# Kernel tuning notes

Measured on AMD Instinct MI355X. Metric: run time of the kernel, lower is better.

Reference implementation:

```python
import jax, jax.numpy as jnp
import numpy as np

H = 128          # hid_feats
IN0, IN1 = 128, 64
OUT = 64         # out_feats
L = 3            # num_layers
N = 50000        # nodes per graph


def _rbf(x, W, b):
    # sklearn RBFSampler: z = sqrt(2/D) * cos(x @ W + b)
    return jnp.sqrt(2.0 / H) * jnp.cos(x @ W + b)


def _sage_branch(feat, src, dst, Wself, Wneigh, bias, n_nodes):
    # deg of each dst node (constant across layers)
    deg = jax.ops.segment_sum(jnp.ones_like(dst, dtype=feat.dtype), dst, n_nodes)
    denom = jnp.maximum(deg, 1.0)[:, None]
    for i in range(Wself.shape[0]):
        s = jax.ops.segment_sum(feat[src], dst, n_nodes)   # gather + scatter-add
        neigh = jnp.where(deg[:, None] > 0, s / denom, 0.0)
        feat = feat @ Wself[i] + neigh @ Wneigh[i] + bias[i]
    return feat


def setup_inputs() -> dict:
    key = jax.random.key(0)
    ks = jax.random.split(key, 20)
    gamma = 0.1
    inp = {}
    inp['feat0'] = jax.random.normal(ks[0], (N, IN0), jnp.float32)
    inp['feat1'] = jax.random.normal(ks[1], (N, IN1), jnp.float32)
    E = 800000
    inp['src0'] = jax.random.randint(ks[2], (E,), 0, N, jnp.int32)
    inp['dst0'] = jax.random.randint(ks[3], (E,), 0, N, jnp.int32)
    inp['src1'] = jax.random.randint(ks[4], (E,), 0, N, jnp.int32)
    inp['dst1'] = jax.random.randint(ks[5], (E,), 0, N, jnp.int32)
    # RBF random Fourier feature params (W ~ sqrt(2*gamma)*N(0,1), b ~ U[0,2pi))
    inp['rbf_W0'] = jnp.sqrt(2 * gamma) * jax.random.normal(ks[6], (IN0, H), jnp.float32)
    inp['rbf_b0'] = jax.random.uniform(ks[7], (H,), jnp.float32, 0.0, 2 * np.pi)
    inp['rbf_W1'] = jnp.sqrt(2 * gamma) * jax.random.normal(ks[8], (IN1, H), jnp.float32)
    inp['rbf_b1'] = jax.random.uniform(ks[9], (H,), jnp.float32, 0.0, 2 * np.pi)
    sc = 1.0 / np.sqrt(H)
    # branch 1 (g1) and branch 2 (g0) SAGEConv params, stacked over layers
    inp['Wself1'] = sc * jax.random.normal(ks[10], (L, H, H), jnp.float32)
    inp['Wneigh1'] = sc * jax.random.normal(ks[11], (L, H, H), jnp.float32)
    inp['b1'] = jnp.zeros((L, H), jnp.float32)
    inp['Wself2'] = sc * jax.random.normal(ks[12], (L, H, H), jnp.float32)
    inp['Wneigh2'] = sc * jax.random.normal(ks[13], (L, H, H), jnp.float32)
    inp['b2'] = jnp.zeros((L, H), jnp.float32)
    inp['fc1_W'] = sc * jax.random.normal(ks[14], (2 * H, H), jnp.float32)
    inp['fc1_b'] = jnp.zeros((H,), jnp.float32)
    inp['out_W'] = sc * jax.random.normal(ks[15], (H, OUT), jnp.float32)
    inp['out_b'] = jnp.zeros((OUT,), jnp.float32)
    inp['ro_W'] = (1.0 / np.sqrt(OUT)) * jax.random.normal(ks[16], (OUT, 1), jnp.float32)
    inp['ro_b'] = jnp.zeros((1,), jnp.float32)
    return inp


def reference(feat0, feat1, src0, dst0, src1, dst1,
              rbf_W0, rbf_b0, rbf_W1, rbf_b1,
              Wself1, Wneigh1, b1, Wself2, Wneigh2, b2,
              fc1_W, fc1_b, out_W, out_b, ro_W, ro_b):
    # branch 1: g1 path-complex features
    h1 = _rbf(feat1, rbf_W1, rbf_b1)
    y1 = _sage_branch(h1, src1, dst1, Wself1, Wneigh1, b1, feat1.shape[0])
    # branch 2: g0 node features
    h0 = _rbf(feat0, rbf_W0, rbf_b0)
    y2 = _sage_branch(h0, src0, dst0, Wself2, Wneigh2, b2, feat0.shape[0])
    # adaptive_avg_pool1d to 1 == mean over nodes
    y = jnp.concatenate([y2.mean(axis=0), y1.mean(axis=0)], axis=0)  # [2H]
    h = jax.nn.relu(y @ fc1_W + fc1_b)          # dropout is identity in eval
    h = jax.nn.leaky_relu(h @ out_W + out_b, negative_slope=0.01)
    return h @ ro_W + ro_b                      # [1]
```

## Files before the change

kernel.cpp:

```cpp
#include <hip/hip_runtime.h>
#include <math.h>

#define HF   128
#define CAPW 64
#define HB   64

__global__ __launch_bounds__(256) void histgemm_kernel(const float* __restrict__ A,
                                                       const float* __restrict__ W,
                                                       const float* __restrict__ bias,
                                                       float* __restrict__ hout,
                                                       float* __restrict__ partial,
                                                       const int* __restrict__ s0, const int* __restrict__ d0,
                                                       const int* __restrict__ s1, const int* __restrict__ d1,
                                                       unsigned int* __restrict__ cntbuf,
                                                       int N, int E, int histBlocks){
  __shared__ __align__(16) unsigned int sm32[6272];

  const int t = threadIdx.x;
  const int HW = (N + 3) >> 2;
  const int HN = ((N + 7) >> 3) << 2;
  const int W0 = HN >> 2;

  if ((int)blockIdx.x < histBlocks){
    const int bid = blockIdx.x;
    const int b  = bid & 63;
    const int br = (bid >> 6) & 1;
    const int z  = bid >> 7;
    const int* keys = z ? (br ? d1 : d0) : (br ? s1 : s0);
    const int C  = (E + HB - 1) / HB;
    const int lo = b * C;
    int hi = lo + C; if (hi > E) hi = E;
    unsigned int* out = cntbuf + ((size_t)(z * 2 + br) * HB + b) * HW;
    #pragma unroll
    for (int h = 0; h < 2; ++h){
      const int klo = h ? HN : 0;
      const int khi = h ? N : HN;
      const int nw = (khi - klo + 3) >> 2;
      for (int w = t; w < nw; w += 256) sm32[w] = 0u;
      __syncthreads();
      for (int i = lo + t; i < hi; i += 256){
        int k = keys[i];
        if (k >= klo && k < khi){
          int kl = k - klo;
          atomicAdd(&sm32[kl >> 2], 1u << ((kl & 3) << 3));
        }
      }
      __syncthreads();
      for (int w = t; w < nw; w += 256) out[h * W0 + w] = sm32[w];
      __syncthreads();
    }
    return;
  }

  float (*As)[68]   = (float(*)[68])sm32;
  float (*Bs)[132]  = (float(*)[132])((float*)sm32 + 1088);
  float (*red)[128] = (float(*)[128])sm32;
  const int tx = t & 15;
  const int ty = t >> 4;
  const int rb = (int)blockIdx.x - histBlocks;
  const int rowbase = rb << 6;

  float acc[4][8];
  #pragma unroll
  for (int i = 0; i < 4; ++i)
    #pragma unroll
    for (int j = 0; j < 8; ++j) acc[i][j] = 0.f;

  const int ar = t >> 2;
  const int ac = (t & 3) << 2;
  const int arow = rowbase + ar;
  const int bk0 = t >> 5;
  const int bc0 = (t & 31) << 2;

  for (int k0 = 0; k0 < 128; k0 += 16){
    __syncthreads();
    float4 av = make_float4(0.f, 0.f, 0.f, 0.f);
    if (arow < N) av = *(const float4*)&A[(size_t)arow * 128 + (k0 + ac)];
    As[ac + 0][ar] = av.x; As[ac + 1][ar] = av.y;
    As[ac + 2][ar] = av.z; As[ac + 3][ar] = av.w;
    float4 b0 = *(const float4*)&W[(size_t)(k0 + bk0) * HF + bc0];
    float4 b1 = *(const float4*)&W[(size_t)(k0 + bk0 + 8) * HF + bc0];
    *(float4*)&Bs[bk0][bc0]     = b0;
    *(float4*)&Bs[bk0 + 8][bc0] = b1;
    __syncthreads();
    #pragma unroll
    for (int kk = 0; kk < 16; ++kk){
      const float4 a  = *(const float4*)&As[kk][ty << 2];
      const float4 p0 = *(const float4*)&Bs[kk][tx << 2];
      const float4 p1 = *(const float4*)&Bs[kk][64 + (tx << 2)];
      const float aa[4] = {a.x, a.y, a.z, a.w};
      const float bb[8] = {p0.x, p0.y, p0.z, p0.w, p1.x, p1.y, p1.z, p1.w};
      #pragma unroll
      for (int i = 0; i < 4; ++i)
        #pragma unroll
        for (int j = 0; j < 8; ++j)
          acc[i][j] = fmaf(aa[i], bb[j], acc[i][j]);
    }
  }

  const float4 bia0 = *(const float4*)&bias[tx << 2];
  const float4 bia1 = *(const float4*)&bias[64 + (tx << 2)];
  const float bb0[8] = {bia0.x, bia0.y, bia0.z, bia0.w, bia1.x, bia1.y, bia1.z, bia1.w};
  float o[4][8];
  float cw[8];
  #pragma unroll
  for (int j = 0; j < 8; ++j) cw[j] = 0.f;
  #pragma unroll
  for (int i = 0; i < 4; ++i){
    int row = rowbase + (ty << 2) + i;
    bool valid = row < N;
    #pragma unroll
    for (int j = 0; j < 8; ++j){
      o[i][j] = 0.125f * cosf(acc[i][j] + bb0[j]);
      if (valid) cw[j] += o[i][j];
    }
    if (valid){
      *(float4*)&hout[(size_t)row * HF + (tx << 2)]      = make_float4(o[i][0], o[i][1], o[i][2], o[i][3]);
      *(float4*)&hout[(size_t)row * HF + 64 + (tx << 2)] = make_float4(o[i][4], o[i][5], o[i][6], o[i][7]);
    }
  }

  __syncthreads();
  #pragma unroll
  for (int j = 0; j < 4; ++j){
    red[ty][(tx << 2) + j]      = cw[j];
    red[ty][64 + (tx << 2) + j] = cw[4 + j];
  }
  __syncthreads();
  for (int off = 8; off; off >>= 1){
    if (ty < off){
      #pragma unroll
      for (int j = 0; j < 4; ++j){
        red[ty][(tx << 2) + j]      += red[ty + off][(tx << 2) + j];
        red[ty][64 + (tx << 2) + j] += red[ty + off][64 + (tx << 2) + j];
      }
    }
    __syncthreads();
  }
  if (ty == 0){
    #pragma unroll
    for (int j = 0; j < 4; ++j){
      partial[(size_t)rb * 512 + (tx << 2) + j]      = red[0][(tx << 2) + j];
      partial[(size_t)rb * 512 + 64 + (tx << 2) + j] = red[0][64 + (tx << 2) + j];
    }
  }
}

__global__ __launch_bounds__(256) void scan_kernel(unsigned int* __restrict__ cntbuf,
                                                   int* __restrict__ deg,
                                                   int* __restrict__ fill, int N){
  int k = blockIdx.x * 256 + threadIdx.x;
  if (k >= 2 * N) return;
  const int br = k >= N;
  const int kk = k - br * N;
  const int HW = (N + 3) >> 2;
  unsigned char* cb = (unsigned char*)cntbuf;
  size_t dbase = ((size_t)(2 + br) * HB) * HW * 4 + kk;
  int ds = 0;
  for (int b = 0; b < HB; ++b) ds += cb[dbase + (size_t)b * HW * 4];
  deg[k] = ds;
  size_t sbase = ((size_t)(0 + br) * HB) * HW * 4 + kk;
  int run = 0;
  for (int b = 0; b < HB; ++b){
    size_t a = sbase + (size_t)b * HW * 4;
    int c = cb[a];
    cb[a] = (unsigned char)run;
    run += c;
  }
  fill[k] = run;
}

__global__ __launch_bounds__(256) void scatter_kernel(const int* __restrict__ s0, const int* __restrict__ d0,
                                                      const int* __restrict__ s1, const int* __restrict__ d1,
                                                      const unsigned int* __restrict__ cntbuf,
                                                      unsigned short* __restrict__ slots,
                                                      int N, int E){
  __shared__ unsigned int sm32[12544];
  const int t  = threadIdx.x;
  const int b  = blockIdx.x & 63;
  const int br = blockIdx.x >> 6;
  const int HW = (N + 3) >> 2;
  const unsigned int* offw = cntbuf + ((size_t)br * HB + b) * HW;
  for (int w = t; w < HW; w += 256) sm32[w] = offw[w];
  __syncthreads();
  const int* srcA = br ? s1 : s0;
  const int* dstA = br ? d1 : d0;
  const int C  = (E + HB - 1) / HB;
  const int lo = b * C;
  int hi = lo + C; if (hi > E) hi = E;
  const size_t obase = (size_t)br * N;
  for (int i = lo + t; i < hi; i += 256){
    int s = srcA[i];
    int d = dstA[i];
    unsigned int old = atomicAdd(&sm32[s >> 2], 1u << ((s & 3) << 3));
    int j = (old >> ((s & 3) << 3)) & 0xff;
    if (j < CAPW) slots[(obase + s) * CAPW + j] = (unsigned short)d;
  }
}

__global__ __launch_bounds__(256) void pull1_kernel(const unsigned short* __restrict__ slots,
                                                    const int* __restrict__ fill,
                                                    const int* __restrict__ deg,
                                                    float* __restrict__ w1,
                                                    float* __restrict__ qa,
                                                    double* __restrict__ S, int N){
  int i = blockIdx.x * 256 + threadIdx.x;
  int t = threadIdx.x;
  float a = 0.f;
  int dgi = 0;
  int br = 0;
  bool valid = i < 2 * N;
  if (valid){
    br = i >= N;
    int o = br * N;
    int c = fill[i]; if (c > CAPW) c = CAPW;
    const unsigned short* sl = slots + (size_t)i * CAPW;
    int j = 0;
    for (; j + 7 < c; j += 8){
      int dA = sl[j], dB = sl[j+1], dC = sl[j+2], dD = sl[j+3];
      int dE = sl[j+4], dF = sl[j+5], dG = sl[j+6], dH = sl[j+7];
      a += 1.f/(float)deg[o+dA] + 1.f/(float)deg[o+dB]
         + 1.f/(float)deg[o+dC] + 1.f/(float)deg[o+dD]
         + 1.f/(float)deg[o+dE] + 1.f/(float)deg[o+dF]
         + 1.f/(float)deg[o+dG] + 1.f/(float)deg[o+dH];
    }
    for (; j < c; ++j) a += 1.f/(float)deg[o + sl[j]];
    dgi = deg[i];
    w1[i] = a;
    qa[i] = dgi > 0 ? a * (1.f/(float)dgi) : 0.f;
  }
  __shared__ double rd[4][256];
  bool pos = valid && dgi > 0;
  rd[0][t] = (pos && !br) ? 1.0 : 0.0;
  rd[1][t] = (pos && !br) ? (double)a : 0.0;
  rd[2][t] = (pos &&  br) ? 1.0 : 0.0;
  rd[3][t] = (pos &&  br) ? (double)a : 0.0;
  __syncthreads();
  for (int off = 128; off; off >>= 1){
    if (t < off){
      rd[0][t] += rd[0][t+off]; rd[1][t] += rd[1][t+off];
      rd[2][t] += rd[2][t+off]; rd[3][t] += rd[3][t+off];
    }
    __syncthreads();
  }
  if (t < 4) atomicAdd(&S[t], rd[t][0]);
}

template<bool WQ>
__global__ __launch_bounds__(256) void pull_kernel(const unsigned short* __restrict__ slots,
                                                   const int* __restrict__ fill,
                                                   const int* __restrict__ deg,
                                                   const float* __restrict__ qin,
                                                   float* __restrict__ wout,
                                                   float* __restrict__ qout, int N){
  int i = blockIdx.x * 256 + threadIdx.x;
  if (i >= 2 * N) return;
  int br = i >= N;
  int o = br * N;
  int c = fill[i]; if (c > CAPW) c = CAPW;
  const unsigned short* sl = slots + (size_t)i * CAPW;
  float a = 0.f;
  int j = 0;
  for (; j + 7 < c; j += 8){
    int dA = sl[j], dB = sl[j+1], dC = sl[j+2], dD = sl[j+3];
    int dE = sl[j+4], dF = sl[j+5], dG = sl[j+6], dH = sl[j+7];
    a += qin[o+dA] + qin[o+dB] + qin[o+dC] + qin[o+dD]
       + qin[o+dE] + qin[o+dF] + qin[o+dG] + qin[o+dH];
  }
  for (; j < c; ++j) a += qin[o + sl[j]];
  wout[i] = a;
  if (WQ){
    int dgi = deg[i];
    qout[i] = dgi > 0 ? a * (1.f/(float)dgi) : 0.f;
  }
}

__global__ __launch_bounds__(256) void tail_kernel(const float* __restrict__ A1,
                                                   const float* __restrict__ W1,
                                                   const float* __restrict__ bias1,
                                                   const float* __restrict__ h0,
                                                   const float* __restrict__ w1,
                                                   const float* __restrict__ w2,
                                                   const float* __restrict__ w3,
                                                   float* __restrict__ partial0,
                                                   float* __restrict__ partial1,
                                                   int N, int gg){
  __shared__ __align__(16) float smem[3200];
  float (*As)[68]   = (float(*)[68])smem;
  float (*Bs)[132]  = (float(*)[132])(smem + 1088);
  float (*red)[128] = (float(*)[128])smem;
  const int t  = threadIdx.x;
  const int tx = t & 15;
  const int ty = t >> 4;

  if ((int)blockIdx.x >= gg){
    const int wb = blockIdx.x - gg;
    const int rowbase = wb << 6;
    float o[4][8];
    float wr[3][4];
    #pragma unroll
    for (int i = 0; i < 4; ++i){
      int row = rowbase + (ty << 2) + i;
      bool valid = row < N;
      float4 x0 = make_float4(0,0,0,0), x1 = make_float4(0,0,0,0);
      if (valid){
        x0 = *(const float4*)&h0[(size_t)row * HF + (tx << 2)];
        x1 = *(const float4*)&h0[(size_t)row * HF + 64 + (tx << 2)];
      }
      o[i][0]=x0.x; o[i][1]=x0.y; o[i][2]=x0.z; o[i][3]=x0.w;
      o[i][4]=x1.x; o[i][5]=x1.y; o[i][6]=x1.z; o[i][7]=x1.w;
      wr[0][i] = valid ? w1[row] : 0.f;
      wr[1][i] = valid ? w2[row] : 0.f;
      wr[2][i] = valid ? w3[row] : 0.f;
    }
    #pragma unroll
    for (int k = 0; k < 3; ++k){
      float cw[8];
      #pragma unroll
      for (int j = 0; j < 8; ++j)
        cw[j] = wr[k][0]*o[0][j] + wr[k][1]*o[1][j] + wr[k][2]*o[2][j] + wr[k][3]*o[3][j];
      __syncthreads();
      #pragma unroll
      for (int j = 0; j < 4; ++j){
        red[ty][(tx << 2) + j]      = cw[j];
        red[ty][64 + (tx << 2) + j] = cw[4 + j];
      }
      __syncthreads();
      for (int off = 8; off; off >>= 1){
        if (ty < off){
          #pragma unroll
          for (int j = 0; j < 4; ++j){
            red[ty][(tx << 2) + j]      += red[ty + off][(tx << 2) + j];
            red[ty][64 + (tx << 2) + j] += red[ty + off][64 + (tx << 2) + j];
          }
        }
        __syncthreads();
      }
      if (ty == 0){
        #pragma unroll
        for (int j = 0; j < 4; ++j){
          partial0[(size_t)wb * 512 + (k + 1) * 128 + (tx << 2) + j]      = red[0][(tx << 2) + j];
          partial0[(size_t)wb * 512 + (k + 1) * 128 + 64 + (tx << 2) + j] = red[0][64 + (tx << 2) + j];
        }
      }
      __syncthreads();
    }
    return;
  }

  const int rowbase = (int)blockIdx.x << 6;
  float acc[4][8];
  #pragma unroll
  for (int i = 0; i < 4; ++i)
    #pragma unroll
    for (int j = 0; j < 8; ++j) acc[i][j] = 0.f;

  const int ar = t >> 2;
  const int ac = (t & 3) << 2;
  const int arow = rowbase + ar;
  const int bk0 = t >> 5;
  const int bc0 = (t & 31) << 2;

  for (int k0 = 0; k0 < 64; k0 += 16){
    __syncthreads();
    float4 av = make_float4(0.f, 0.f, 0.f, 0.f);
    if (arow < N) av = *(const float4*)&A1[(size_t)arow * 64 + (k0 + ac)];
    As[ac + 0][ar] = av.x; As[ac + 1][ar] = av.y;
    As[ac + 2][ar] = av.z; As[ac + 3][ar] = av.w;
    float4 b0 = *(const float4*)&W1[(size_t)(k0 + bk0) * HF + bc0];
    float4 b1 = *(const float4*)&W1[(size_t)(k0 + bk0 + 8) * HF + bc0];
    *(float4*)&Bs[bk0][bc0]     = b0;
    *(float4*)&Bs[bk0 + 8][bc0] = b1;
    __syncthreads();
    #pragma unroll
    for (int kk = 0; kk < 16; ++kk){
      const float4 a  = *(const float4*)&As[kk][ty << 2];
      const float4 p0 = *(const float4*)&Bs[kk][tx << 2];
      const float4 p1 = *(const float4*)&Bs[kk][64 + (tx << 2)];
      const float aa[4] = {a.x, a.y, a.z, a.w};
      const float bb[8] = {p0.x, p0.y, p0.z, p0.w, p1.x, p1.y, p1.z, p1.w};
      #pragma unroll
      for (int i = 0; i < 4; ++i)
        #pragma unroll
        for (int j = 0; j < 8; ++j)
          acc[i][j] = fmaf(aa[i], bb[j], acc[i][j]);
    }
  }

  const float4 bia0 = *(const float4*)&bias1[tx << 2];
  const float4 bia1 = *(const float4*)&bias1[64 + (tx << 2)];
  const float bb0[8] = {bia0.x, bia0.y, bia0.z, bia0.w, bia1.x, bia1.y, bia1.z, bia1.w};
  float o[4][8];
  float wr[4][4];
  #pragma unroll
  for (int i = 0; i < 4; ++i){
    int row = rowbase + (ty << 2) + i;
    bool valid = row < N;
    #pragma unroll
    for (int j = 0; j < 8; ++j)
      o[i][j] = 0.125f * cosf(acc[i][j] + bb0[j]);
    wr[0][i] = valid ? 1.f : 0.f;
    wr[1][i] = valid ? w1[N + row] : 0.f;
    wr[2][i] = valid ? w2[N + row] : 0.f;
    wr[3][i] = valid ? w3[N + row] : 0.f;
  }
  __syncthreads();
  #pragma unroll
  for (int k = 0; k < 4; ++k){
    float cw[8];
    #pragma unroll
    for (int j = 0; j < 8; ++j)
      cw[j] = wr[k][0]*o[0][j] + wr[k][1]*o[1][j] + wr[k][2]*o[2][j] + wr[k][3]*o[3][j];
    #pragma unroll
    for (int j = 0; j < 4; ++j){
      red[ty][(tx << 2) + j]      = cw[j];
      red[ty][64 + (tx << 2) + j] = cw[4 + j];
    }
    __syncthreads();
    for (int off = 8; off; off >>= 1){
      if (ty < off){
        #pragma unroll
        for (int j = 0; j < 4; ++j){
          red[ty][(tx << 2) + j]      += red[ty + off][(tx << 2) + j];
          red[ty][64 + (tx << 2) + j] += red[ty + off][64 + (tx << 2) + j];
        }
      }
      __syncthreads();
    }
    if (ty == 0){
      #pragma unroll
      for (int j = 0; j < 4; ++j){
        partial1[(size_t)blockIdx.x * 512 + k * 128 + (tx << 2) + j]      = red[0][(tx << 2) + j];
        partial1[(size_t)blockIdx.x * 512 + k * 128 + 64 + (tx << 2) + j] = red[0][64 + (tx << 2) + j];
      }
    }
    __syncthreads();
  }
}

__global__ __launch_bounds__(512) void greduce_kernel(const float* __restrict__ partial,
                                                      double* __restrict__ G, int nb, int stride){
  int br = blockIdx.y;
  const float* p = partial + (size_t)br * stride;
  double* Gb = G + 512 * br;
  int t = threadIdx.x;
  double s = 0.0;
  for (int b = blockIdx.x; b < nb; b += gridDim.x) s += (double)p[(size_t)b * 512 + t];
  atomicAdd(&Gb[t], s);
}

__global__ __launch_bounds__(512) void head_kernel(const double* __restrict__ G,
                                                   const double* __restrict__ S,
                                                   const float* __restrict__ WsA, const float* __restrict__ WnA, const float* __restrict__ bA,
                                                   const float* __restrict__ WsB, const float* __restrict__ WnB, const float* __restrict__ bB,
                                                   float* __restrict__ ymean, int n){
  const int br = blockIdx.x;
  const double* Gb = G + 512 * br;
  const double* Sb = S + 2 * br;
  const float* Ws   = br ? WsB : WsA;
  const float* Wn   = br ? WnB : WnA;
  const float* bias = br ? bB  : bA;
  float* yout = ymean + 128 * br;

  __shared__ double g[4][128], ng[3][128];
  __shared__ float lws[32][128], lwn[32][128];
  const int t = threadIdx.x;
  const int k = t >> 7, j = t & 127;
  g[k][j] = Gb[t];
  double s[4];
  s[0] = (double)n; s[1] = Sb[0]; s[2] = Sb[1]; s[3] = 0.0;

  for (int i = 0; i < 3; ++i){
    const float* ws = Ws + (size_t)i * 16384;
    const float* wn = Wn + (size_t)i * 16384;
    const float* bi = bias + (size_t)i * 128;
    const int kmax = 2 - i;
    double a = (k <= kmax) ? s[k] * (double)bi[j] : 0.0;
    for (int mc = 0; mc < 128; mc += 32){
      __syncthreads();
      #pragma unroll
      for (int pp = 0; pp < 2; ++pp){
        int idx = (pp * 512 + t) << 2;
        int mm = idx >> 7, cc = idx & 127;
        *(float4*)&lws[mm][cc] = *(const float4*)&ws[(size_t)(mc + mm) * 128 + cc];
        *(float4*)&lwn[mm][cc] = *(const float4*)&wn[(size_t)(mc + mm) * 128 + cc];
      }
      __syncthreads();
      if (k <= kmax){
        #pragma unroll
        for (int m = 0; m < 32; ++m){
          a += g[k][mc + m]     * (double)lws[m][j];
          a += g[k + 1][mc + m] * (double)lwn[m][j];
        }
      }
    }
    __syncthreads();
    if (k <= kmax) ng[k][j] = a;
    __syncthreads();
    if (k <= kmax) g[k][j] = ng[k][j];
  }
  __syncthreads();
  if (t < 128) yout[t] = (float)(g[0][t] / (double)n);
}

__global__ void final_kernel(const float* __restrict__ ymean,
                             const float* __restrict__ fc1W, const float* __restrict__ fc1b,
                             const float* __restrict__ outW, const float* __restrict__ outb,
                             const float* __restrict__ roW, const float* __restrict__ rob,
                             float* __restrict__ out){
  __shared__ float y[256], h1[128], h2[64];
  int t = threadIdx.x;
  y[t] = ymean[t];
  __syncthreads();
  if (t < 128){
    float a = fc1b[t];
    for (int k = 0; k < 256; ++k) a = fmaf(y[k], fc1W[k * 128 + t], a);
    h1[t] = a > 0.f ? a : 0.f;
  }
  __syncthreads();
  if (t < 64){
    float a = outb[t];
    for (int k = 0; k < 128; ++k) a = fmaf(h1[k], outW[k * 64 + t], a);
    h2[t] = a > 0.f ? a : 0.01f * a;
  }
  __syncthreads();
  if (t == 0){
    float a = rob[0];
    for (int k = 0; k < 64; ++k) a = fmaf(h2[k], roW[k], a);
    out[0] = a;
  }
}

extern "C" void kernel_launch(void* const* d_in, const int* in_sizes, int n_in,
                              void* d_out, int out_size, void* d_ws, size_t ws_size,
                              hipStream_t stream){
  const float* feat0  = (const float*)d_in[0];
  const float* feat1  = (const float*)d_in[1];
  const int*   src0   = (const int*)d_in[2];
  const int*   dst0   = (const int*)d_in[3];
  const int*   src1   = (const int*)d_in[4];
  const int*   dst1   = (const int*)d_in[5];
  const float* rbfW0  = (const float*)d_in[6];
  const float* rbfb0  = (const float*)d_in[7];
  const float* rbfW1  = (const float*)d_in[8];
  const float* rbfb1  = (const float*)d_in[9];
  const float* Wself1 = (const float*)d_in[10];
  const float* Wneigh1= (const float*)d_in[11];
  const float* b1     = (const float*)d_in[12];
  const float* Wself2 = (const float*)d_in[13];
  const float* Wneigh2= (const float*)d_in[14];
  const float* b2     = (const float*)d_in[15];
  const float* fc1W   = (const float*)d_in[16];
  const float* fc1b   = (const float*)d_in[17];
  const float* outW   = (const float*)d_in[18];
  const float* outb   = (const float*)d_in[19];
  const float* roW    = (const float*)d_in[20];
  const float* rob    = (const float*)d_in[21];

  const int N = in_sizes[0] / 128;
  const int E = in_sizes[2];
  const int HW = (N + 3) >> 2;

  char* w = (char*)d_ws;
  size_t off = 0;
  auto alloc = [&](size_t bytes) -> char* {
    char* p = w + off; off += (bytes + 255) & ~(size_t)255; return p;
  };
  int*    deg    = (int*)   alloc((size_t)2 * N * 4);
  int*    fill   = (int*)   alloc((size_t)2 * N * 4);
  float*  w1     = (float*) alloc((size_t)2 * N * 4);
  float*  w2     = (float*) alloc((size_t)2 * N * 4);
  float*  w3     = (float*) alloc((size_t)2 * N * 4);
  float*  qa     = (float*) alloc((size_t)2 * N * 4);
  float*  qb     = (float*) alloc((size_t)2 * N * 4);
  double* S      = (double*)alloc(4 * sizeof(double));
  double* G      = (double*)alloc(1024 * sizeof(double));
  float*  ymean  = (float*) alloc(256 * sizeof(float));
  const int gg   = (N + 63) >> 6;
  float*  partial= (float*) alloc((size_t)2 * gg * 512 * 4);
  float*  h0buf  = (float*) alloc((size_t)N * HF * 4);
  unsigned short* slots = (unsigned short*)alloc((size_t)2 * N * CAPW * 2);
  unsigned int* cntbuf  = (unsigned int*)alloc((size_t)4 * HB * HW * 4);

  const size_t slen = (size_t)((char*)ymean - (char*)S);

  const int nGrid2 = (2 * N + 255) >> 8;

  hipMemsetAsync(S, 0, slen, stream);
  histgemm_kernel<<<256 + gg, 256, 0, stream>>>(feat0, rbfW0, rbfb0, h0buf, partial,
                                                src0, dst0, src1, dst1, cntbuf, N, E, 256);
  scan_kernel<<<nGrid2, 256, 0, stream>>>(cntbuf, deg, fill, N);
  scatter_kernel<<<128, 256, 0, stream>>>(src0, dst0, src1, dst1, cntbuf, slots, N, E);
  pull1_kernel<<<nGrid2, 256, 0, stream>>>(slots, fill, deg, w1, qa, S, N);
  pull_kernel<true ><<<nGrid2, 256, 0, stream>>>(slots, fill, deg, qa, w2, qb, N);
  pull_kernel<false><<<nGrid2, 256, 0, stream>>>(slots, fill, deg, qb, w3, qb, N);
  tail_kernel<<<2 * gg, 256, 0, stream>>>(feat1, rbfW1, rbfb1, h0buf, w1, w2, w3,
                                          partial, partial + (size_t)gg * 512, N, gg);
  greduce_kernel<<<dim3(16, 2), 512, 0, stream>>>(partial, G, gg, gg * 512);
  head_kernel<<<2, 512, 0, stream>>>(G, S, Wself2, Wneigh2, b2, Wself1, Wneigh1, b1, ymean, N);
  final_kernel<<<1, 256, 0, stream>>>(ymean, fc1W, fc1b, outW, outb, roW, rob, (float*)d_out);
}
```

Baseline: 212.7 us.

## Split RBF GEMM into thirds co-scheduled with pull phases; single-pass histogram

```diff
diff --git a/kernel.cpp b/kernel.cpp
--- a/kernel.cpp
+++ b/kernel.cpp
@@ -5,150 +5,38 @@
 #define CAPW 64
 #define HB   64
 
-__global__ __launch_bounds__(256) void histgemm_kernel(const float* __restrict__ A,
-                                                       const float* __restrict__ W,
-                                                       const float* __restrict__ bias,
-                                                       float* __restrict__ hout,
-                                                       float* __restrict__ partial,
-                                                       const int* __restrict__ s0, const int* __restrict__ d0,
-                                                       const int* __restrict__ s1, const int* __restrict__ d1,
-                                                       unsigned int* __restrict__ cntbuf,
-                                                       int N, int E, int histBlocks){
-  __shared__ __align__(16) unsigned int sm32[6272];
-
+__global__ __launch_bounds__(256) void hist_kernel(const int* __restrict__ s0, const int* __restrict__ d0,
+                                                   const int* __restrict__ s1, const int* __restrict__ d1,
+                                                   unsigned int* __restrict__ cntbuf,
+                                                   int N, int E){
+  __shared__ unsigned int sm32[12544];
   const int t = threadIdx.x;
   const int HW = (N + 3) >> 2;
-  const int HN = ((N + 7) >> 3) << 2;
-  const int W0 = HN >> 2;
-
-  if ((int)blockIdx.x < histBlocks){
-    const int bid = blockIdx.x;
-    const int b  = bid & 63;
-    const int br = (bid >> 6) & 1;
-    const int z  = bid >> 7;
-    const int* keys = z ? (br ? d1 : d0) : (br ? s1 : s0);
-    const int C  = (E + HB - 1) / HB;
-    const int lo = b * C;
-    int hi = lo + C; if (hi > E) hi = E;
-    unsigned int* out = cntbuf + ((size_t)(z * 2 + br) * HB + b) * HW;
-    #pragma unroll
-    for (int h = 0; h < 2; ++h){
-      const int klo = h ? HN : 0;
-      const int khi = h ? N : HN;
-      const int nw = (khi - klo + 3) >> 2;
-      for (int w = t; w < nw; w += 256) sm32[w] = 0u;
-      __syncthreads();
-      for (int i = lo + t; i < hi; i += 256){
-        int k = keys[i];
-        if (k >= klo && k < khi){
-          int kl = k - klo;
-          atomicAdd(&sm32[kl >> 2], 1u << ((kl & 3) << 3));
-        }
-      }
-      __syncthreads();
-      for (int w = t; w < nw; w += 256) out[h * W0 + w] = sm32[w];
-      __syncthreads();
-    }
-    return;
-  }
-
-  float (*As)[68]   = (float(*)[68])sm32;
-  float (*Bs)[132]  = (float(*)[132])((float*)sm32 + 1088);
-  float (*red)[128] = (float(*)[128])sm32;
-  const int tx = t & 15;
-  const int ty = t >> 4;
-  const int rb = (int)blockIdx.x - histBlocks;
-  const int rowbase = rb << 6;
-
-  float acc[4][8];
-  #pragma unroll
-  for (int i = 0; i < 4; ++i)
-    #pragma unroll
-    for (int j = 0; j < 8; ++j) acc[i][j] = 0.f;
-
-  const int ar = t >> 2;
-  const int ac = (t & 3) << 2;
-  const int arow = rowbase + ar;
-  const int bk0 = t >> 5;
-  const int bc0 = (t & 31) << 2;
-
-  for (int k0 = 0; k0 < 128; k0 += 16){
-    __syncthreads();
-    float4 av = make_float4(0.f, 0.f, 0.f, 0.f);
-    if (arow < N) av = *(const float4*)&A[(size_t)arow * 128 + (k0 + ac)];
-    As[ac + 0][ar] = av.x; As[ac + 1][ar] = av.y;
-    As[ac + 2][ar] = av.z; As[ac + 3][ar] = av.w;
-    float4 b0 = *(const float4*)&W[(size_t)(k0 + bk0) * HF + bc0];
-    float4 b1 = *(const float4*)&W[(size_t)(k0 + bk0 + 8) * HF + bc0];
-    *(float4*)&Bs[bk0][bc0]     = b0;
-    *(float4*)&Bs[bk0 + 8][bc0] = b1;
-    __syncthreads();
-    #pragma unroll
-    for (int kk = 0; kk < 16; ++kk){
-      const float4 a  = *(const float4*)&As[kk][ty << 2];
-      const float4 p0 = *(const float4*)&Bs[kk][tx << 2];
-      const float4 p1 = *(const float4*)&Bs[kk][64 + (tx << 2)];
-      const float aa[4] = {a.x, a.y, a.z, a.w};
-      const float bb[8] = {p0.x, p0.y, p0.z, p0.w, p1.x, p1.y, p1.z, p1.w};
-      #pragma unroll
-      for (int i = 0; i < 4; ++i)
-        #pragma unroll
-        for (int j = 0; j < 8; ++j)
-          acc[i][j] = fmaf(aa[i], bb[j], acc[i][j]);
-    }
-  }
-
-  const float4 bia0 = *(const float4*)&bias[tx << 2];
-  const float4 bia1 = *(const float4*)&bias[64 + (tx << 2)];
-  const float bb0[8] = {bia0.x, bia0.y, bia0.z, bia0.w, bia1.x, bia1.y, bia1.z, bia1.w};
-  float o[4][8];
-  float cw[8];
-  #pragma unroll
-  for (int j = 0; j < 8; ++j) cw[j] = 0.f;
-  #pragma unroll
-  for (int i = 0; i < 4; ++i){
-    int row = rowbase + (ty << 2) + i;
-    bool valid = row < N;
-    #pragma unroll
-    for (int j = 0; j < 8; ++j){
-      o[i][j] = 0.125f * cosf(acc[i][j] + bb0[j]);
-      if (valid) cw[j] += o[i][j];
-    }
-    if (valid){
-      *(float4*)&hout[(size_t)row * HF + (tx << 2)]      = make_float4(o[i][0], o[i][1], o[i][2], o[i][3]);
-      *(float4*)&hout[(size_t)row * HF + 64 + (tx << 2)] = make_float4(o[i][4], o[i][5], o[i][6], o[i][7]);
-    }
-  }
-
-  __syncthreads();
-  #pragma unroll
-  for (int j = 0; j < 4; ++j){
-    red[ty][(tx << 2) + j]      = cw[j];
-    red[ty][64 + (tx << 2) + j] = cw[4 + j];
-  }
-  __syncthreads();
-  for (int off = 8; off; off >>= 1){
-    if (ty < off){
-      #pragma unroll
-      for (int j = 0; j < 4; ++j){
-        red[ty][(tx << 2) + j]      += red[ty + off][(tx << 2) + j];
-        red[ty][64 + (tx << 2) + j] += red[ty + off][64 + (tx << 2) + j];
-      }
-    }
-    __syncthreads();
-  }
-  if (ty == 0){
-    #pragma unroll
-    for (int j = 0; j < 4; ++j){
-      partial[(size_t)rb * 512 + (tx << 2) + j]      = red[0][(tx << 2) + j];
-      partial[(size_t)rb * 512 + 64 + (tx << 2) + j] = red[0][64 + (tx << 2) + j];
-    }
-  }
+  const int b  = blockIdx.x & 63;
+  const int br = (blockIdx.x >> 6) & 1;
+  const int z  = blockIdx.x >> 7;
+  const int* keys = z ? (br ? d1 : d0) : (br ? s1 : s0);
+  for (int w = t; w < HW; w += 256) sm32[w] = 0u;
+  __syncthreads();
+  const int C  = (E + HB - 1) / HB;
+  const int lo = b * C;
+  int hi = lo + C; if (hi > E) hi = E;
+  for (int i = lo + t; i < hi; i += 256){
+    int k = keys[i];
+    atomicAdd(&sm32[k >> 2], 1u << ((k & 3) << 3));
+  }
+  __syncthreads();
+  unsigned int* out = cntbuf + ((size_t)(z * 2 + br) * HB + b) * HW;
+  for (int w = t; w < HW; w += 256) out[w] = sm32[w];
 }
 
 __global__ __launch_bounds__(256) void scan_kernel(unsigned int* __restrict__ cntbuf,
                                                    int* __restrict__ deg,
-                                                   int* __restrict__ fill, int N){
+                                                   int* __restrict__ fill,
+                                                   double* __restrict__ SG, int N){
+  if (blockIdx.x == 0){
+    for (int z = threadIdx.x; z < 1056; z += 256) SG[z] = 0.0;
+  }
   int k = blockIdx.x * 256 + threadIdx.x;
   if (k >= 2 * N) return;
   const int br = k >= N;
@@ -175,13 +63,18 @@
                                                       const unsigned int* __restrict__ cntbuf,
                                                       unsigned short* __restrict__ slots,
                                                       int N, int E){
-  __shared__ unsigned int sm32[12544];
+  __shared__ unsigned int sm32[6272];
   const int t  = threadIdx.x;
   const int b  = blockIdx.x & 63;
-  const int br = blockIdx.x >> 6;
+  const int br = (blockIdx.x >> 6) & 1;
+  const int h  = blockIdx.x >> 7;
   const int HW = (N + 3) >> 2;
-  const unsigned int* offw = cntbuf + ((size_t)br * HB + b) * HW;
-  for (int w = t; w < HW; w += 256) sm32[w] = offw[w];
+  const int HN = ((N + 7) >> 3) << 2;
+  const int klo = h ? HN : 0;
+  const int khi = h ? N : HN;
+  const int nw  = (khi - klo + 3) >> 2;
+  const unsigned int* offw = cntbuf + ((size_t)br * HB + b) * HW + (klo >> 2);
+  for (int w = t; w < nw; w += 256) sm32[w] = offw[w];
   __syncthreads();
   const int* srcA = br ? s1 : s0;
   const int* dstA = br ? d1 : d0;
@@ -191,88 +84,208 @@
   const size_t obase = (size_t)br * N;
   for (int i = lo + t; i < hi; i += 256){
     int s = srcA[i];
+    if (s < klo || s >= khi) continue;
     int d = dstA[i];
-    unsigned int old = atomicAdd(&sm32[s >> 2], 1u << ((s & 3) << 3));
-    int j = (old >> ((s & 3) << 3)) & 0xff;
+    int sl = s - klo;
+    unsigned int old = atomicAdd(&sm32[sl >> 2], 1u << ((sl & 3) << 3));
+    int j = (old >> ((sl & 3) << 3)) & 0xff;
     if (j < CAPW) slots[(obase + s) * CAPW + j] = (unsigned short)d;
   }
 }
 
-__global__ __launch_bounds__(256) void pull1_kernel(const unsigned short* __restrict__ slots,
-                                                    const int* __restrict__ fill,
-                                                    const int* __restrict__ deg,
-                                                    float* __restrict__ w1,
-                                                    float* __restrict__ qa,
-                                                    double* __restrict__ S, int N){
-  int i = blockIdx.x * 256 + threadIdx.x;
-  int t = threadIdx.x;
-  float a = 0.f;
-  int dgi = 0;
-  int br = 0;
-  bool valid = i < 2 * N;
-  if (valid){
-    br = i >= N;
-    int o = br * N;
-    int c = fill[i]; if (c > CAPW) c = CAPW;
-    const unsigned short* sl = slots + (size_t)i * CAPW;
-    int j = 0;
-    for (; j + 7 < c; j += 8){
-      int dA = sl[j], dB = sl[j+1], dC = sl[j+2], dD = sl[j+3];
-      int dE = sl[j+4], dF = sl[j+5], dG = sl[j+6], dH = sl[j+7];
-      a += 1.f/(float)deg[o+dA] + 1.f/(float)deg[o+dB]
-         + 1.f/(float)deg[o+dC] + 1.f/(float)deg[o+dD]
-         + 1.f/(float)deg[o+dE] + 1.f/(float)deg[o+dF]
-         + 1.f/(float)deg[o+dG] + 1.f/(float)deg[o+dH];
-    }
-    for (; j < c; ++j) a += 1.f/(float)deg[o + sl[j]];
-    dgi = deg[i];
-    w1[i] = a;
-    qa[i] = dgi > 0 ? a * (1.f/(float)dgi) : 0.f;
-  }
-  __shared__ double rd[4][256];
-  bool pos = valid && dgi > 0;
-  rd[0][t] = (pos && !br) ? 1.0 : 0.0;
-  rd[1][t] = (pos && !br) ? (double)a : 0.0;
-  rd[2][t] = (pos &&  br) ? 1.0 : 0.0;
-  rd[3][t] = (pos &&  br) ? (double)a : 0.0;
-  __syncthreads();
-  for (int off = 128; off; off >>= 1){
-    if (t < off){
-      rd[0][t] += rd[0][t+off]; rd[1][t] += rd[1][t+off];
-      rd[2][t] += rd[2][t+off]; rd[3][t] += rd[3][t+off];
-    }
-    __syncthreads();
-  }
-  if (t < 4) atomicAdd(&S[t], rd[t][0]);
-}
-
-template<bool WQ>
-__global__ __launch_bounds__(256) void pull_kernel(const unsigned short* __restrict__ slots,
-                                                   const int* __restrict__ fill,
-                                                   const int* __restrict__ deg,
-                                                   const float* __restrict__ qin,
-                                                   float* __restrict__ wout,
-                                                   float* __restrict__ qout, int N){
-  int i = blockIdx.x * 256 + threadIdx.x;
-  if (i >= 2 * N) return;
-  int br = i >= N;
-  int o = br * N;
-  int c = fill[i]; if (c > CAPW) c = CAPW;
-  const unsigned short* sl = slots + (size_t)i * CAPW;
-  float a = 0.f;
-  int j = 0;
-  for (; j + 7 < c; j += 8){
-    int dA = sl[j], dB = sl[j+1], dC = sl[j+2], dD = sl[j+3];
-    int dE = sl[j+4], dF = sl[j+5], dG = sl[j+6], dH = sl[j+7];
-    a += qin[o+dA] + qin[o+dB] + qin[o+dC] + qin[o+dD]
-       + qin[o+dE] + qin[o+dF] + qin[o+dG] + qin[o+dH];
-  }
-  for (; j < c; ++j) a += qin[o + sl[j]];
-  wout[i] = a;
-  if (WQ){
-    int dgi = deg[i];
-    qout[i] = dgi > 0 ? a * (1.f/(float)dgi) : 0.f;
-  }
+__device__ __forceinline__ void gemmacc128(const float* __restrict__ A,
+                                           const float* __restrict__ W,
+                                           const float* __restrict__ bias,
+                                           float* __restrict__ h0,
+                                           float* __restrict__ partial,
+                                           int rb, int N, float* smemf){
+  float (*As)[68]   = (float(*)[68])smemf;
+  float (*Bs)[132]  = (float(*)[132])(smemf + 2176);
+  float (*red)[128] = (float(*)[128])smemf;
+  const int t  = threadIdx.x;
+  const int tx = t & 15;
+  const int ty = t >> 4;
+  const int rowbase = rb << 6;
+
+  float acc[4][8];
+  #pragma unroll
+  for (int i = 0; i < 4; ++i)
+    #pragma unroll
+    for (int j = 0; j < 8; ++j) acc[i][j] = 0.f;
+
+  const int ar = t >> 2;
+  const int ac = (t & 3) << 2;
+  const int arow = rowbase + ar;
+  const int bk0 = t >> 5;
+  const int bc0 = (t & 31) << 2;
+
+  for (int k0 = 0; k0 < 128; k0 += 32){
+    __syncthreads();
+    float4 av0 = make_float4(0.f,0.f,0.f,0.f), av1 = make_float4(0.f,0.f,0.f,0.f);
+    if (arow < N){
+      av0 = *(const float4*)&A[(size_t)arow * 128 + (k0 + ac)];
+      av1 = *(const float4*)&A[(size_t)arow * 128 + (k0 + 16 + ac)];
+    }
+    As[ac + 0][ar]      = av0.x; As[ac + 1][ar]      = av0.y;
+    As[ac + 2][ar]      = av0.z; As[ac + 3][ar]      = av0.w;
+    As[16 + ac + 0][ar] = av1.x; As[16 + ac + 1][ar] = av1.y;
+    As[16 + ac + 2][ar] = av1.z; As[16 + ac + 3][ar] = av1.w;
+    #pragma unroll
+    for (int r = 0; r < 4; ++r)
+      *(float4*)&Bs[bk0 + 8*r][bc0] =
+        *(const float4*)&W[(size_t)(k0 + bk0 + 8*r) * HF + bc0];
+    __syncthreads();
+    #pragma unroll
+    for (int kk = 0; kk < 32; ++kk){
+      const float4 a  = *(const float4*)&As[kk][ty << 2];
+      const float4 p0 = *(const float4*)&Bs[kk][tx << 2];
+      const float4 p1 = *(const float4*)&Bs[kk][64 + (tx << 2)];
+      const float aa[4] = {a.x, a.y, a.z, a.w};
+      const float bb[8] = {p0.x, p0.y, p0.z, p0.w, p1.x, p1.y, p1.z, p1.w};
+      #pragma unroll
+      for (int i = 0; i < 4; ++i)
+        #pragma unroll
+        for (int j = 0; j < 8; ++j)
+          acc[i][j] = fmaf(aa[i], bb[j], acc[i][j]);
+    }
+  }
+
+  const float4 bia0 = *(const float4*)&bias[tx << 2];
+  const float4 bia1 = *(const float4*)&bias[64 + (tx << 2)];
+  const float bb0[8] = {bia0.x, bia0.y, bia0.z, bia0.w, bia1.x, bia1.y, bia1.z, bia1.w};
+  float o[4][8];
+  float cw[8];
+  #pragma unroll
+  for (int j = 0; j < 8; ++j) cw[j] = 0.f;
+  #pragma unroll
+  for (int i = 0; i < 4; ++i){
+    int row = rowbase + (ty << 2) + i;
+    bool valid = row < N;
+    #pragma unroll
+    for (int j = 0; j < 8; ++j){
+      o[i][j] = 0.125f * __cosf(acc[i][j] + bb0[j]);
+      if (valid) cw[j] += o[i][j];
+    }
+    if (valid){
+      *(float4*)&h0[(size_t)row * HF + (tx << 2)]      = make_float4(o[i][0], o[i][1], o[i][2], o[i][3]);
+      *(float4*)&h0[(size_t)row * HF + 64 + (tx << 2)] = make_float4(o[i][4], o[i][5], o[i][6], o[i][7]);
+    }
+  }
+  __syncthreads();
+  #pragma unroll
+  for (int j = 0; j < 4; ++j){
+    red[ty][(tx << 2) + j]      = cw[j];
+    red[ty][64 + (tx << 2) + j] = cw[4 + j];
+  }
+  __syncthreads();
+  for (int off = 8; off; off >>= 1){
+    if (ty < off){
+      #pragma unroll
+      for (int j = 0; j < 4; ++j){
+        red[ty][(tx << 2) + j]      += red[ty + off][(tx << 2) + j];
+        red[ty][64 + (tx << 2) + j] += red[ty + off][64 + (tx << 2) + j];
+      }
+    }
+    __syncthreads();
+  }
+  if (ty == 0){
+    #pragma unroll
+    for (int j = 0; j < 4; ++j){
+      partial[(size_t)rb * 512 + (tx << 2) + j]      = red[0][(tx << 2) + j];
+      partial[(size_t)rb * 512 + 64 + (tx << 2) + j] = red[0][64 + (tx << 2) + j];
+    }
+  }
+}
+
+template<int PHASE>
+__global__ __launch_bounds__(256) void pullgemm_kernel(const float* __restrict__ A0,
+                                                       const float* __restrict__ W0,
+                                                       const float* __restrict__ b0,
+                                                       const unsigned short* __restrict__ slots,
+                                                       const int* __restrict__ fill,
+                                                       const int* __restrict__ deg,
+                                                       float* __restrict__ w1, float* __restrict__ qa,
+                                                       float* __restrict__ qb,
+                                                       float* __restrict__ w2, float* __restrict__ w3,
+                                                       double* __restrict__ S,
+                                                       float* __restrict__ h0,
+                                                       float* __restrict__ partial,
+                                                       int N, int gbase, int pullBlocks){
+  __shared__ __align__(16) float smem[6400];
+  const int t = threadIdx.x;
+
+  if ((int)blockIdx.x < pullBlocks){
+    int i = blockIdx.x * 256 + t;
+    if (PHASE == 1){
+      float a = 0.f;
+      int dgi = 0, br = 0;
+      bool valid = i < 2 * N;
+      if (valid){
+        br = i >= N;
+        int o = br * N;
+        int c = fill[i]; if (c > CAPW) c = CAPW;
+        const unsigned short* sl = slots + (size_t)i * CAPW;
+        int j = 0;
+        for (; j + 7 < c; j += 8){
+          int dA = sl[j], dB = sl[j+1], dC = sl[j+2], dD = sl[j+3];
+          int dE = sl[j+4], dF = sl[j+5], dG = sl[j+6], dH = sl[j+7];
+          a += 1.f/(float)deg[o+dA] + 1.f/(float)deg[o+dB]
+             + 1.f/(float)deg[o+dC] + 1.f/(float)deg[o+dD]
+             + 1.f/(float)deg[o+dE] + 1.f/(float)deg[o+dF]
+             + 1.f/(float)deg[o+dG] + 1.f/(float)deg[o+dH];
+        }
+        for (; j < c; ++j) a += 1.f/(float)deg[o + sl[j]];
+        dgi = deg[i];
+        w1[i] = a;
+        qa[i] = dgi > 0 ? a * (1.f/(float)dgi) : 0.f;
+      }
+      double* rd = (double*)smem;
+      bool pos = valid && dgi > 0;
+      rd[0*256+t] = (pos && !br) ? 1.0 : 0.0;
+      rd[1*256+t] = (pos && !br) ? (double)a : 0.0;
+      rd[2*256+t] = (pos &&  br) ? 1.0 : 0.0;
+      rd[3*256+t] = (pos &&  br) ? (double)a : 0.0;
+      __syncthreads();
+      for (int off = 128; off; off >>= 1){
+        if (t < off){
+          rd[t]       += rd[t+off];
+          rd[256+t]   += rd[256+t+off];
+          rd[512+t]   += rd[512+t+off];
+          rd[768+t]   += rd[768+t+off];
+        }
+        __syncthreads();
+      }
+      if (t < 4) atomicAdd(&S[t], rd[t*256]);
+      return;
+    } else {
+      if (i >= 2 * N) return;
+      int br = i >= N;
+      int o = br * N;
+      int c = fill[i]; if (c > CAPW) c = CAPW;
+      const unsigned short* sl = slots + (size_t)i * CAPW;
+      const float* qin = (PHASE == 2) ? qa : qb;
+      float a = 0.f;
+      int j = 0;
+      for (; j + 7 < c; j += 8){
+        int dA = sl[j], dB = sl[j+1], dC = sl[j+2], dD = sl[j+3];
+        int dE = sl[j+4], dF = sl[j+5], dG = sl[j+6], dH = sl[j+7];
+        a += qin[o+dA] + qin[o+dB] + qin[o+dC] + qin[o+dD]
+           + qin[o+dE] + qin[o+dF] + qin[o+dG] + qin[o+dH];
+      }
+      for (; j < c; ++j) a += qin[o + sl[j]];
+      if (PHASE == 2){
+        w2[i] = a;
+        int dgi = deg[i];
+        qb[i] = dgi > 0 ? a * (1.f/(float)dgi) : 0.f;
+      } else {
+        w3[i] = a;
+      }
+      return;
+    }
+  }
+
+  int rb = (int)blockIdx.x - pullBlocks + gbase;
+  gemmacc128(A0, W0, b0, h0, partial, rb, N, smem);
 }
 
 __global__ __launch_bounds__(256) void tail_kernel(const float* __restrict__ A1,
@@ -285,10 +298,11 @@
                                                    float* __restrict__ partial0,
                                                    float* __restrict__ partial1,
                                                    int N, int gg){
-  __shared__ __align__(16) float smem[3200];
+  __shared__ __align__(16) float smem[6400];
   float (*As)[68]   = (float(*)[68])smem;
-  float (*Bs)[132]  = (float(*)[132])(smem + 1088);
-  float (*red)[128] = (float(*)[128])smem;
+  float (*Bs)[132]  = (float(*)[132])(smem + 2176);
+  float (*red)[256] = (float(*)[256])smem;
+  float (*red1)[128]= (float(*)[128])smem;
   const int t  = threadIdx.x;
   const int tx = t & 15;
   const int ty = t >> 4;
@@ -322,16 +336,16 @@
       __syncthreads();
       #pragma unroll
       for (int j = 0; j < 4; ++j){
-        red[ty][(tx << 2) + j]      = cw[j];
-        red[ty][64 + (tx << 2) + j] = cw[4 + j];
+        red1[ty][(tx << 2) + j]      = cw[j];
+        red1[ty][64 + (tx << 2) + j] = cw[4 + j];
       }
       __syncthreads();
       for (int off = 8; off; off >>= 1){
         if (ty < off){
           #pragma unroll
           for (int j = 0; j < 4; ++j){
-            red[ty][(tx << 2) + j]      += red[ty + off][(tx << 2) + j];
-            red[ty][64 + (tx << 2) + j] += red[ty + off][64 + (tx << 2) + j];
+            red1[ty][(tx << 2) + j]      += red1[ty + off][(tx << 2) + j];
+            red1[ty][64 + (tx << 2) + j] += red1[ty + off][64 + (tx << 2) + j];
           }
         }
         __syncthreads();
@@ -339,8 +353,8 @@
       if (ty == 0){
         #pragma unroll
         for (int j = 0; j < 4; ++j){
-          partial0[(size_t)wb * 512 + (k + 1) * 128 + (tx << 2) + j]      = red[0][(tx << 2) + j];
-          partial0[(size_t)wb * 512 + (k + 1) * 128 + 64 + (tx << 2) + j] = red[0][64 + (tx << 2) + j];
+          partial0[(size_t)wb * 512 + (k + 1) * 128 + (tx << 2) + j]      = red1[0][(tx << 2) + j];
+          partial0[(size_t)wb * 512 + (k + 1) * 128 + 64 + (tx << 2) + j] = red1[0][64 + (tx << 2) + j];
         }
       }
       __syncthreads();
@@ -348,7 +362,8 @@
     return;
   }
 
-  const int rowbase = (int)blockIdx.x << 6;
+  const int rb = (int)blockIdx.x;
+  const int rowbase = rb << 6;
   float acc[4][8];
   #pragma unroll
   for (int i = 0; i < 4; ++i)
@@ -361,19 +376,24 @@
   const int bk0 = t >> 5;
   const int bc0 = (t & 31) << 2;
 
-  for (int k0 = 0; k0 < 64; k0 += 16){
-    __syncthreads();
-    float4 av = make_float4(0.f, 0.f, 0.f, 0.f);
-    if (arow < N) av = *(const float4*)&A1[(size_t)arow * 64 + (k0 + ac)];
-    As[ac + 0][ar] = av.x; As[ac + 1][ar] = av.y;
-    As[ac + 2][ar] = av.z; As[ac + 3][ar] = av.w;
-    float4 b0 = *(const float4*)&W1[(size_t)(k0 + bk0) * HF + bc0];
-    float4 b1 = *(const float4*)&W1[(size_t)(k0 + bk0 + 8) * HF + bc0];
-    *(float4*)&Bs[bk0][bc0]     = b0;
-    *(float4*)&Bs[bk0 + 8][bc0] = b1;
-    __syncthreads();
-    #pragma unroll
-    for (int kk = 0; kk < 16; ++kk){
+  for (int k0 = 0; k0 < 64; k0 += 32){
+    __syncthreads();
+    float4 av0 = make_float4(0.f,0.f,0.f,0.f), av1 = make_float4(0.f,0.f,0.f,0.f);
+    if (arow < N){
+      av0 = *(const float4*)&A1[(size_t)arow * 64 + (k0 + ac)];
+      av1 = *(const float4*)&A1[(size_t)arow * 64 + (k0 + 16 + ac)];
+    }
+    As[ac + 0][ar]      = av0.x; As[ac + 1][ar]      = av0.y;
+    As[ac + 2][ar]      = av0.z; As[ac + 3][ar]      = av0.w;
+    As[16 + ac + 0][ar] = av1.x; As[16 + ac + 1][ar] = av1.y;
+    As[16 + ac + 2][ar] = av1.z; As[16 + ac + 3][ar] = av1.w;
+    #pragma unroll
+    for (int r = 0; r < 4; ++r)
+      *(float4*)&Bs[bk0 + 8*r][bc0] =
+        *(const float4*)&W1[(size_t)(k0 + bk0 + 8*r) * HF + bc0];
+    __syncthreads();
+    #pragma unroll
+    for (int kk = 0; kk < 32; ++kk){
       const float4 a  = *(const float4*)&As[kk][ty << 2];
       const float4 p0 = *(const float4*)&Bs[kk][tx << 2];
       const float4 p1 = *(const float4*)&Bs[kk][64 + (tx << 2)];
@@ -398,7 +418,7 @@
     bool valid = row < N;
     #pragma unroll
     for (int j = 0; j < 8; ++j)
-      o[i][j] = 0.125f * cosf(acc[i][j] + bb0[j]);
+      o[i][j] = 0.125f * __cosf(acc[i][j] + bb0[j]);
     wr[0][i] = valid ? 1.f : 0.f;
     wr[1][i] = valid ? w1[N + row] : 0.f;
     wr[2][i] = valid ? w2[N + row] : 0.f;
@@ -406,23 +426,30 @@
   }
   __syncthreads();
   #pragma unroll
-  for (int k = 0; k < 4; ++k){
-    float cw[8];
-    #pragma unroll
-    for (int j = 0; j < 8; ++j)
-      cw[j] = wr[k][0]*o[0][j] + wr[k][1]*o[1][j] + wr[k][2]*o[2][j] + wr[k][3]*o[3][j];
+  for (int kp = 0; kp < 2; ++kp){
+    const int kA = kp * 2, kB = kp * 2 + 1;
+    float cwA[8], cwB[8];
+    #pragma unroll
+    for (int j = 0; j < 8; ++j){
+      cwA[j] = wr[kA][0]*o[0][j] + wr[kA][1]*o[1][j] + wr[kA][2]*o[2][j] + wr[kA][3]*o[3][j];
+      cwB[j] = wr[kB][0]*o[0][j] + wr[kB][1]*o[1][j] + wr[kB][2]*o[2][j] + wr[kB][3]*o[3][j];
+    }
     #pragma unroll
     for (int j = 0; j < 4; ++j){
-      red[ty][(tx << 2) + j]      = cw[j];
-      red[ty][64 + (tx << 2) + j] = cw[4 + j];
+      red[ty][(tx << 2) + j]        = cwA[j];
+      red[ty][64 + (tx << 2) + j]   = cwA[4 + j];
+      red[ty][128 + (tx << 2) + j]  = cwB[j];
+      red[ty][192 + (tx << 2) + j]  = cwB[4 + j];
     }
     __syncthreads();
     for (int off = 8; off; off >>= 1){
       if (ty < off){
         #pragma unroll
         for (int j = 0; j < 4; ++j){
-          red[ty][(tx << 2) + j]      += red[ty + off][(tx << 2) + j];
-          red[ty][64 + (tx << 2) + j] += red[ty + off][64 + (tx << 2) + j];
+          red[ty][(tx << 2) + j]       += red[ty + off][(tx << 2) + j];
+          red[ty][64 + (tx << 2) + j]  += red[ty + off][64 + (tx << 2) + j];
+          red[ty][128 + (tx << 2) + j] += red[ty + off][128 + (tx << 2) + j];
+          red[ty][192 + (tx << 2) + j] += red[ty + off][192 + (tx << 2) + j];
         }
       }
       __syncthreads();
@@ -430,8 +457,10 @@
     if (ty == 0){
       #pragma unroll
       for (int j = 0; j < 4; ++j){
-        partial1[(size_t)blockIdx.x * 512 + k * 128 + (tx << 2) + j]      = red[0][(tx << 2) + j];
-        partial1[(size_t)blockIdx.x * 512 + k * 128 + 64 + (tx << 2) + j] = red[0][64 + (tx << 2) + j];
+        partial1[(size_t)rb * 512 + kA * 128 + (tx << 2) + j]      = red[0][(tx << 2) + j];
+        partial1[(size_t)rb * 512 + kA * 128 + 64 + (tx << 2) + j] = red[0][64 + (tx << 2) + j];
+        partial1[(size_t)rb * 512 + kB * 128 + (tx << 2) + j]      = red[0][128 + (tx << 2) + j];
+        partial1[(size_t)rb * 512 + kB * 128 + 64 + (tx << 2) + j] = red[0][192 + (tx << 2) + j];
       }
     }
     __syncthreads();
@@ -582,18 +611,23 @@
   unsigned short* slots = (unsigned short*)alloc((size_t)2 * N * CAPW * 2);
   unsigned int* cntbuf  = (unsigned int*)alloc((size_t)4 * HB * HW * 4);
 
-  const size_t slen = (size_t)((char*)ymean - (char*)S);
-
   const int nGrid2 = (2 * N + 255) >> 8;
-
-  hipMemsetAsync(S, 0, slen, stream);
-  histgemm_kernel<<<256 + gg, 256, 0, stream>>>(feat0, rbfW0, rbfb0, h0buf, partial,
-                                                src0, dst0, src1, dst1, cntbuf, N, E, 256);
-  scan_kernel<<<nGrid2, 256, 0, stream>>>(cntbuf, deg, fill, N);
-  scatter_kernel<<<128, 256, 0, stream>>>(src0, dst0, src1, dst1, cntbuf, slots, N, E);
-  pull1_kernel<<<nGrid2, 256, 0, stream>>>(slots, fill, deg, w1, qa, S, N);
-  pull_kernel<true ><<<nGrid2, 256, 0, stream>>>(slots, fill, deg, qa, w2, qb, N);
-  pull_kernel<false><<<nGrid2, 256, 0, stream>>>(slots, fill, deg, qb, w3, qb, N);
+  const int ch = (gg + 2) / 3;
+  const int c0 = 0, c1 = ch, c2 = 2 * ch;
+  const int n0 = ch, n1 = (2*ch > gg ? gg - ch : ch), n2 = gg - 2 * ch;
+
+  hist_kernel<<<256, 256, 0, stream>>>(src0, dst0, src1, dst1, cntbuf, N, E);
+  scan_kernel<<<nGrid2, 256, 0, stream>>>(cntbuf, deg, fill, S, N);
+  scatter_kernel<<<256, 256, 0, stream>>>(src0, dst0, src1, dst1, cntbuf, slots, N, E);
+  pullgemm_kernel<1><<<nGrid2 + n0, 256, 0, stream>>>(feat0, rbfW0, rbfb0, slots, fill, deg,
+                                                      w1, qa, qb, w2, w3, S, h0buf, partial,
+                                                      N, c0, nGrid2);
+  pullgemm_kernel<2><<<nGrid2 + n1, 256, 0, stream>>>(feat0, rbfW0, rbfb0, slots, fill, deg,
+                                                      w1, qa, qb, w2, w3, S, h0buf, partial,
+                                                      N, c1, nGrid2);
+  pullgemm_kernel<3><<<nGrid2 + n2, 256, 0, stream>>>(feat0, rbfW0, rbfb0, slots, fill, deg,
+                                                      w1, qa, qb, w2, w3, S, h0buf, partial,
+                                                      N, c2, nGrid2);
   tail_kernel<<<2 * gg, 256, 0, stream>>>(feat1, rbfW1, rbfb1, h0buf, w1, w2, w3,
                                           partial, partial + (size_t)gg * 512, N, gg);
   greduce_kernel<<<dim3(16, 2), 512, 0, stream>>>(partial, G, gg, gg * 512);
```

Measured after the change: 204.9 us. -3.6%, faster.
